# Optimization experiments

Hardware: AMD Instinct MI355X
Metric: run time of the kernel (lower is better)

## Reference

```python
import jax, jax.numpy as jnp
import numpy as np
import math

B, SES, SEQ, H, K = 16, 16, 64, 512, 32
L = SES * SEQ


def setup_inputs() -> dict:
    key = jax.random.key(0)
    ks = jax.random.split(key, 16)
    s = 1.0 / math.sqrt(H)
    return {
        "user_emb": jax.random.normal(ks[0], (B, H), jnp.float32),
        "item_emb": jax.random.normal(ks[1], (B, SES, SEQ, H), jnp.float32),
        "mask": jnp.zeros((B, L, K), jnp.float32),
        "index": jax.random.randint(ks[2], (L, K), 0, L, jnp.int64),
        "Wq": jax.random.normal(ks[3], (H, H), jnp.float32) * s,
        "bq": jnp.zeros((H,), jnp.float32),
        "Wk": jax.random.normal(ks[4], (H, H), jnp.float32) * s,
        "bk": jnp.zeros((H,), jnp.float32),
        "Wv": jax.random.normal(ks[5], (H, H), jnp.float32) * s,
        "bv": jnp.zeros((H,), jnp.float32),
        "Wd": jax.random.normal(ks[6], (H, H), jnp.float32) * s,
        "bd": jnp.zeros((H,), jnp.float32),
        "ln_g": jnp.ones((H,), jnp.float32),
        "ln_b": jnp.zeros((H,), jnp.float32),
    }


def reference(user_emb, item_emb, mask, index, Wq, bq, Wk, bk, Wv, bv, Wd, bd, ln_g, ln_b):
    b, ses, seq, h = item_emb.shape
    l = ses * seq
    item_flat = item_emb.reshape(b, l, h)
    q = user_emb @ Wq.T + bq                       # [B, H]
    k = item_flat @ Wk.T + bk                      # [B, L, H]
    v = item_flat @ Wv.T + bv                      # [B, L, H]
    # scalar query against all L keys, scaled by sqrt(hidden_size)
    scores = jnp.einsum("bh,blh->bl", q, k) / math.sqrt(h)
    scores = scores[:, index] + mask               # gather -> [B, L, K]
    w = jax.nn.softmax(scores, axis=-1)            # [B, L, K]
    vg = v[:, index, :]                            # gather -> [B, L, K, H]
    attn_out = jnp.einsum("blk,blkh->blh", w, vg)  # [B, L, H]
    dense = attn_out @ Wd.T + bd
    x = dense + item_flat                          # residual (dropout = identity, eval)
    mu = jnp.mean(x, axis=-1, keepdims=True)
    var = jnp.var(x, axis=-1, keepdims=True)
    y = (x - mu) / jnp.sqrt(var + 1e-12) * ln_g + ln_b
    return y.reshape(b, ses, seq, h)
```

## Files before the change

kernel.cpp:

```cpp
#include <hip/hip_runtime.h>
#include <math.h>

constexpr int HD   = 512;
constexpr int LL   = 1024;
constexpr int MT   = 16384;
constexpr int KNBR = 32;
constexpr float SCL = 0.04419417382415922f;

typedef __attribute__((ext_vector_type(8))) short  bf16x8;
typedef __attribute__((ext_vector_type(4))) float  f32x4;
typedef __attribute__((ext_vector_type(8))) unsigned short us8;

__device__ inline float b2f(unsigned short u) {
    union { unsigned int i; float f; } v; v.i = (unsigned int)u << 16; return v.f;
}
__device__ inline float b2f_lo(unsigned int u) {
    union { unsigned int i; float f; } v; v.i = u << 16; return v.f;
}
__device__ inline float b2f_hi(unsigned int u) {
    union { unsigned int i; float f; } v; v.i = u & 0xffff0000u; return v.f;
}
__device__ inline unsigned short f2b(float x) {
    union { float f; unsigned int u; } v; v.f = x;
    unsigned int r = v.u + 0x7fff + ((v.u >> 16) & 1);
    return (unsigned short)(r >> 16);
}

__global__ __launch_bounds__(256) void conv_bf(
    const float* __restrict__ s, unsigned short* __restrict__ d, int n)
{
    const int i = (blockIdx.x * 256 + threadIdx.x) * 4;
    if (i < n) {
        float4 v = *(const float4*)&s[i];
        ushort4 o;
        o.x = f2b(v.x); o.y = f2b(v.y); o.z = f2b(v.z); o.w = f2b(v.w);
        *(ushort4*)&d[i] = o;
    }
}

__global__ __launch_bounds__(256) void conv_w3(
    const float* __restrict__ Wk, const float* __restrict__ Wv,
    const float* __restrict__ Wd, unsigned short* __restrict__ Wkv,
    unsigned short* __restrict__ Wdb)
{
    const int n = HD*HD;
    const int i = (blockIdx.x * 256 + threadIdx.x) * 4;
    const float* s; unsigned short* d; int off;
    if (i < n)            { s = Wk; d = Wkv;     off = i; }
    else if (i < 2*n)     { s = Wv; d = Wkv + n; off = i - n; }
    else                  { s = Wd; d = Wdb;     off = i - 2*n; }
    float4 v = *(const float4*)&s[off];
    ushort4 o;
    o.x = f2b(v.x); o.y = f2b(v.y); o.z = f2b(v.z); o.w = f2b(v.w);
    *(ushort4*)&d[off] = o;
}

__global__ __launch_bounds__(256) void gp_q(
    const float* __restrict__ u, const float* __restrict__ Wq,
    const float* __restrict__ bq, float* __restrict__ q)
{
    const int wid  = blockIdx.x * 4 + (threadIdx.x >> 6);
    const int lane = threadIdx.x & 63;
    const int b = wid >> 9, h = wid & 511;
    const float* ur = &u[b*HD + lane*8];
    const float* wr = &Wq[(size_t)h*HD + lane*8];
    const float4 u0 = *(const float4*)ur,     u1 = *(const float4*)(ur+4);
    const float4 w0 = *(const float4*)wr,     w1 = *(const float4*)(wr+4);
    float acc = u0.x*w0.x + u0.y*w0.y + u0.z*w0.z + u0.w*w0.w
              + u1.x*w1.x + u1.y*w1.y + u1.z*w1.z + u1.w*w1.w;
    #pragma unroll
    for (int off = 32; off; off >>= 1) acc += __shfl_down(acc, off);
    if (lane == 0) q[b*HD + h] = acc + bq[h];
}

__global__ __launch_bounds__(256) void scores_init(
    const float* __restrict__ q, const float* __restrict__ bk,
    float* __restrict__ scores)
{
    const int b = blockIdx.x, tid = threadIdx.x;
    float p = q[b*HD + tid]*bk[tid] + q[b*HD + tid + 256]*bk[tid + 256];
    #pragma unroll
    for (int off = 32; off; off >>= 1) p += __shfl_down(p, off);
    __shared__ float sp[4];
    if ((tid & 63) == 0) sp[tid >> 6] = p;
    __syncthreads();
    const float s = (sp[0] + sp[1] + sp[2] + sp[3]) * SCL;
    float4 o = {s, s, s, s};
    *(float4*)&scores[b*LL + tid*4] = o;
}

__global__ __launch_bounds__(256) void gemm_kv(
    const unsigned short* __restrict__ A, const unsigned short* __restrict__ W,
    const float* __restrict__ q, const float* __restrict__ bv,
    float* __restrict__ scores, unsigned short* __restrict__ v_bf)
{
    __shared__ unsigned short As[128 * 32];
    __shared__ unsigned short Bs[128 * 32];

    const int tid  = threadIdx.x;
    const int wave = tid >> 6, lane = tid & 63;
    const int wm = (wave >> 1) * 64;
    const int wn = (wave & 1)  * 64;
    const int row0 = blockIdx.x * 128;
    const int col0 = blockIdx.y * 128;

    const int lrr = lane >> 2;
    const int cc  = lane & 3;
    int st_row[2], st_gchunk[2];
    #pragma unroll
    for (int t = 0; t < 2; t++) {
        const int m = wave*32 + t*16 + lrr;
        st_row[t]    = m;
        st_gchunk[t] = cc ^ ((m >> 1) & 3);
    }

    const int fr   = lane & 15;
    const int quad = lane >> 4;

    f32x4 acc[4][4];
    #pragma unroll
    for (int i = 0; i < 4; i++)
        #pragma unroll
        for (int j = 0; j < 4; j++)
            acc[i][j] = (f32x4){0.f, 0.f, 0.f, 0.f};

    int a_off[4], b_off[4];
    #pragma unroll
    for (int i = 0; i < 4; i++) {
        const int m = wm + i*16 + fr;
        a_off[i] = m*32 + ((quad ^ ((m >> 1) & 3)) << 3);
        const int n = wn + i*16 + fr;
        b_off[i] = n*32 + ((quad ^ ((n >> 1) & 3)) << 3);
    }

    for (int k0 = 0; k0 < HD; k0 += 32) {
        #pragma unroll
        for (int t = 0; t < 2; t++) {
            const int m = st_row[t];
            const unsigned short* ga = &A[(size_t)(row0 + m)*HD + k0 + st_gchunk[t]*8];
            __builtin_amdgcn_global_load_lds(
                (const __attribute__((address_space(1))) void*)ga,
                (__attribute__((address_space(3))) void*)&As[(wave*32 + t*16)*32],
                16, 0, 0);
            const unsigned short* gw = &W[(size_t)(col0 + m)*HD + k0 + st_gchunk[t]*8];
            __builtin_amdgcn_global_load_lds(
                (const __attribute__((address_space(1))) void*)gw,
                (__attribute__((address_space(3))) void*)&Bs[(wave*32 + t*16)*32],
                16, 0, 0);
        }
        __syncthreads();

        bf16x8 af[4], bfr[4];
        #pragma unroll
        for (int i = 0; i < 4; i++) {
            af[i]  = *(const bf16x8*)&As[a_off[i]];
            bfr[i] = *(const bf16x8*)&Bs[b_off[i]];
        }
        #pragma unroll
        for (int i = 0; i < 4; i++)
            #pragma unroll
            for (int j = 0; j < 4; j++)
                acc[i][j] = __builtin_amdgcn_mfma_f32_16x16x32_bf16(
                    af[i], bfr[j], acc[i][j], 0, 0, 0);
        __syncthreads();
    }

    if (col0 < HD) {
        const int b = row0 >> 10;
        float qv[4];
        #pragma unroll
        for (int j = 0; j < 4; j++)
            qv[j] = q[b*HD + col0 + wn + j*16 + fr];
        #pragma unroll
        for (int i = 0; i < 4; i++) {
            #pragma unroll
            for (int r = 0; r < 4; r++) {
                float p = acc[i][0][r]*qv[0] + acc[i][1][r]*qv[1]
                        + acc[i][2][r]*qv[2] + acc[i][3][r]*qv[3];
                #pragma unroll
                for (int off = 1; off < 16; off <<= 1) p += __shfl_xor(p, off);
                if (fr == 0)
                    atomicAdd(&scores[row0 + wm + i*16 + quad*4 + r], p * SCL);
            }
        }
    } else {
        #pragma unroll
        for (int j = 0; j < 4; j++) {
            const int col = col0 - HD + wn + j*16 + fr;
            const float bb = bv[col];
            #pragma unroll
            for (int i = 0; i < 4; i++) {
                #pragma unroll
                for (int r = 0; r < 4; r++) {
                    const int row = row0 + wm + i*16 + quad*4 + r;
                    v_bf[(size_t)row*HD + col] = f2b(acc[i][j][r] + bb);
                }
            }
        }
    }
}

__global__ __launch_bounds__(256) void gp_attn(
    const float* __restrict__ scores, const int* __restrict__ index,
    const float* __restrict__ mask, const unsigned short* __restrict__ v,
    unsigned short* __restrict__ attn)
{
    const int m = blockIdx.x * 4 + (threadIdx.x >> 6);
    const int lane = threadIdx.x & 63;
    const int b = m >> 10, l = m & 1023;

    const int t = lane & 31;
    const int idx = index[l*KNBR + t];
    const float s = scores[b*LL + idx] + mask[(size_t)m*KNBR + t];

    float mx = s;
    #pragma unroll
    for (int off = 16; off; off >>= 1) mx = fmaxf(mx, __shfl_xor(mx, off));
    const float e = __expf(s - mx);
    float sum = e;
    #pragma unroll
    for (int off = 16; off; off >>= 1) sum += __shfl_xor(sum, off);
    const float w = e / sum;

    const unsigned short* vbase = v + (size_t)(b << 10) * HD + lane*8;
    float a[8] = {};
    #pragma unroll 8
    for (int t2 = 0; t2 < KNBR; t2++) {
        const int   it = __shfl(idx, t2);
        const float wt = __shfl(w,   t2);
        const uint4 pv = *(const uint4*)(vbase + (size_t)it*HD);
        a[0] += wt * b2f_lo(pv.x); a[1] += wt * b2f_hi(pv.x);
        a[2] += wt * b2f_lo(pv.y); a[3] += wt * b2f_hi(pv.y);
        a[4] += wt * b2f_lo(pv.z); a[5] += wt * b2f_hi(pv.z);
        a[6] += wt * b2f_lo(pv.w); a[7] += wt * b2f_hi(pv.w);
    }
    uint4 o;
    o.x = (unsigned int)f2b(a[0]) | ((unsigned int)f2b(a[1]) << 16);
    o.y = (unsigned int)f2b(a[2]) | ((unsigned int)f2b(a[3]) << 16);
    o.z = (unsigned int)f2b(a[4]) | ((unsigned int)f2b(a[5]) << 16);
    o.w = (unsigned int)f2b(a[6]) | ((unsigned int)f2b(a[7]) << 16);
    *(uint4*)&attn[(size_t)m*HD + lane*8] = o;
}

__global__ __launch_bounds__(256) void dense_ln(
    const unsigned short* __restrict__ A,
    const unsigned short* __restrict__ W,
    const float* __restrict__ bd, const unsigned short* __restrict__ res,
    const float* __restrict__ ln_g, const float* __restrict__ ln_b,
    float* __restrict__ out)
{
    __shared__ unsigned short As[32 * 32];
    __shared__ unsigned short Bs[512 * 32];
    __shared__ float g_s[HD], lb_s[HD];
    __shared__ float rsum[4][32], rsq[4][32];

    const int tid  = threadIdx.x;
    const int wave = tid >> 6, lane = tid & 63;
    const int row0 = blockIdx.x * 32;

    {
        const int i = tid * 2;
        *(float2*)&g_s[i]  = *(const float2*)&ln_g[i];
        *(float2*)&lb_s[i] = *(const float2*)&ln_b[i];
    }

    const int lrr = lane >> 2;
    const int cc  = lane & 3;
    const int fr   = lane & 15;
    const int quad = lane >> 4;

    f32x4 acc[2][8];
    #pragma unroll
    for (int i = 0; i < 2; i++)
        #pragma unroll
        for (int j = 0; j < 8; j++)
            acc[i][j] = (f32x4){0.f, 0.f, 0.f, 0.f};

    int a_off[2], b_off[8];
    #pragma unroll
    for (int i = 0; i < 2; i++) {
        const int m = i*16 + fr;
        a_off[i] = m*32 + ((quad ^ ((m >> 1) & 3)) << 3);
    }
    #pragma unroll
    for (int j = 0; j < 8; j++) {
        const int n = wave*128 + j*16 + fr;
        b_off[j] = n*32 + ((quad ^ ((n >> 1) & 3)) << 3);
    }

    for (int k0 = 0; k0 < HD; k0 += 32) {
        #pragma unroll
        for (int t = 0; t < 8; t++) {
            const int n = wave*128 + t*16 + lrr;
            const int gch = cc ^ ((n >> 1) & 3);
            const unsigned short* gw = &W[(size_t)n*HD + k0 + gch*8];
            __builtin_amdgcn_global_load_lds(
                (const __attribute__((address_space(1))) void*)gw,
                (__attribute__((address_space(3))) void*)&Bs[(wave*128 + t*16)*32],
                16, 0, 0);
        }
        if (wave < 2) {
            const int m = wave*16 + lrr;
            const int gch = cc ^ ((m >> 1) & 3);
            const unsigned short* ga = &A[(size_t)(row0 + m)*HD + k0 + gch*8];
            __builtin_amdgcn_global_load_lds(
                (const __attribute__((address_space(1))) void*)ga,
                (__attribute__((address_space(3))) void*)&As[(wave*16)*32],
                16, 0, 0);
        }
        __syncthreads();

        bf16x8 af[2], bfr[8];
        #pragma unroll
        for (int i = 0; i < 2; i++) af[i] = *(const bf16x8*)&As[a_off[i]];
        #pragma unroll
        for (int j = 0; j < 8; j++) bfr[j] = *(const bf16x8*)&Bs[b_off[j]];
        #pragma unroll
        for (int i = 0; i < 2; i++)
            #pragma unroll
            for (int j = 0; j < 8; j++)
                acc[i][j] = __builtin_amdgcn_mfma_f32_16x16x32_bf16(
                    af[i], bfr[j], acc[i][j], 0, 0, 0);
        __syncthreads();
    }

    float bdv[8];
    #pragma unroll
    for (int j = 0; j < 8; j++) bdv[j] = bd[wave*128 + j*16 + fr];

    float s1[2][4], s2[2][4];
    #pragma unroll
    for (int i = 0; i < 2; i++) {
        #pragma unroll
        for (int r = 0; r < 4; r++) {
            const int lrow = i*16 + quad*4 + r;
            const size_t gr = (size_t)(row0 + lrow) * HD;
            float a1 = 0.f, a2 = 0.f;
            #pragma unroll
            for (int j = 0; j < 8; j++) {
                const int col = wave*128 + j*16 + fr;
                float val = acc[i][j][r] + bdv[j] + b2f(res[gr + col]);
                acc[i][j][r] = val;
                a1 += val; a2 += val*val;
            }
            #pragma unroll
            for (int off = 1; off < 16; off <<= 1) {
                a1 += __shfl_xor(a1, off);
                a2 += __shfl_xor(a2, off);
            }
            s1[i][r] = a1; s2[i][r] = a2;
            if (fr == 0) { rsum[wave][lrow] = a1; rsq[wave][lrow] = a2; }
        }
    }
    __syncthreads();

    #pragma unroll
    for (int i = 0; i < 2; i++) {
        #pragma unroll
        for (int r = 0; r < 4; r++) {
            const int lrow = i*16 + quad*4 + r;
            const float tot  = rsum[0][lrow] + rsum[1][lrow] + rsum[2][lrow] + rsum[3][lrow];
            const float tot2 = rsq[0][lrow]  + rsq[1][lrow]  + rsq[2][lrow]  + rsq[3][lrow];
            const float mu  = tot * (1.f/HD);
            const float var = tot2 * (1.f/HD) - mu*mu;
            const float inv = rsqrtf(var + 1e-12f);
            const size_t gr = (size_t)(row0 + lrow) * HD;
            #pragma unroll
            for (int j = 0; j < 8; j++) {
                const int col = wave*128 + j*16 + fr;
                out[gr + col] = (acc[i][j][r] - mu)*inv*g_s[col] + lb_s[col];
            }
        }
    }
}

extern "C" void kernel_launch(void* const* d_in, const int* in_sizes, int n_in,
                              void* d_out, int out_size, void* d_ws, size_t ws_size,
                              hipStream_t stream) {
    const float* user_emb = (const float*)d_in[0];
    const float* item_emb = (const float*)d_in[1];
    const float* mask     = (const float*)d_in[2];
    const int*   index    = (const int*)  d_in[3];
    const float* Wq = (const float*)d_in[4];  const float* bq = (const float*)d_in[5];
    const float* Wk = (const float*)d_in[6];  const float* bk = (const float*)d_in[7];
    const float* Wv = (const float*)d_in[8];  const float* bv = (const float*)d_in[9];
    const float* Wd = (const float*)d_in[10]; const float* bd = (const float*)d_in[11];
    const float* ln_g = (const float*)d_in[12];
    const float* ln_b = (const float*)d_in[13];

    float* out = (float*)d_out;

    char* p = (char*)d_ws;
    unsigned short* item_bf = (unsigned short*)p; p += (size_t)MT*HD*2;
    unsigned short* v_bf    = (unsigned short*)p; p += (size_t)MT*HD*2;
    unsigned short* attn_bf = (unsigned short*)p; p += (size_t)MT*HD*2;
    unsigned short* Wkv_bf  = (unsigned short*)p; p += (size_t)2*HD*HD*2;
    unsigned short* Wd_bf   = (unsigned short*)p; p += (size_t)HD*HD*2;
    float* q      = (float*)p; p += 16*HD*4;
    float* scores = (float*)p; p += MT*4;

    conv_bf<<<MT*HD/4/256, 256, 0, stream>>>(item_emb, item_bf, MT*HD);
    conv_w3<<<3*HD*HD/4/256, 256, 0, stream>>>(Wk, Wv, Wd, Wkv_bf, Wd_bf);

    gp_q<<<2048, 256, 0, stream>>>(user_emb, Wq, bq, q);
    scores_init<<<16, 256, 0, stream>>>(q, bk, scores);

    dim3 gkv(MT/128, 8);
    gemm_kv<<<gkv, 256, 0, stream>>>(item_bf, Wkv_bf, q, bv, scores, v_bf);

    gp_attn<<<MT/4, 256, 0, stream>>>(scores, index, mask, v_bf, attn_bf);

    dense_ln<<<MT/32, 256, 0, stream>>>(attn_bf, Wd_bf, bd, item_bf,
                                        ln_g, ln_b, out);
}
```

Measured before the change: 202.9 us.

## Fuse prep kernels into one launch and fuse gather-attention into dense+LayerNorm

Merges the four setup kernels (item/weight bf16 conversion, q projection, score init) into one launch. The score-init blocks recompute q redundantly so they do not depend on the q blocks in the same launch. The gather-attention output is now computed per 32-row tile straight into shared memory inside the dense+LayerNorm kernel, which removes the attn_bf global round trip and one launch. gemm_kv's grid is transposed so consecutive blocks share the same row tile. In exchange, the fused kernel uses more LDS per block, which may lower occupancy, and the score-init blocks add redundant Wq reads.

```diff
diff --git a/kernel.cpp b/kernel.cpp
--- a/kernel.cpp
+++ b/kernel.cpp
@@ -9,7 +9,6 @@
 
 typedef __attribute__((ext_vector_type(8))) short  bf16x8;
 typedef __attribute__((ext_vector_type(4))) float  f32x4;
-typedef __attribute__((ext_vector_type(8))) unsigned short us8;
 
 __device__ inline float b2f(unsigned short u) {
     union { unsigned int i; float f; } v; v.i = (unsigned int)u << 16; return v.f;
@@ -26,67 +25,86 @@
     return (unsigned short)(r >> 16);
 }
 
-__global__ __launch_bounds__(256) void conv_bf(
-    const float* __restrict__ s, unsigned short* __restrict__ d, int n)
+constexpr int PB_CONV_I = 8192;
+constexpr int PB_CONV_W = 768;
+constexpr int PB_Q      = 2048;
+constexpr int PB_SINIT  = 16;
+
+__global__ __launch_bounds__(256) void prep(
+    const float* __restrict__ item, const float* __restrict__ Wk,
+    const float* __restrict__ Wv, const float* __restrict__ Wd,
+    const float* __restrict__ u, const float* __restrict__ Wq,
+    const float* __restrict__ bq, const float* __restrict__ bk,
+    unsigned short* __restrict__ item_bf, unsigned short* __restrict__ Wkv_bf,
+    unsigned short* __restrict__ Wd_bf, float* __restrict__ q,
+    float* __restrict__ scores)
 {
-    const int i = (blockIdx.x * 256 + threadIdx.x) * 4;
-    if (i < n) {
-        float4 v = *(const float4*)&s[i];
+    const int blk = blockIdx.x, tid = threadIdx.x;
+
+    if (blk < PB_CONV_I) {
+        const int i = blk * 1024 + tid * 4;
+        float4 v = *(const float4*)&item[i];
         ushort4 o;
         o.x = f2b(v.x); o.y = f2b(v.y); o.z = f2b(v.z); o.w = f2b(v.w);
-        *(ushort4*)&d[i] = o;
-    }
-}
-
-__global__ __launch_bounds__(256) void conv_w3(
-    const float* __restrict__ Wk, const float* __restrict__ Wv,
-    const float* __restrict__ Wd, unsigned short* __restrict__ Wkv,
-    unsigned short* __restrict__ Wdb)
-{
-    const int n = HD*HD;
-    const int i = (blockIdx.x * 256 + threadIdx.x) * 4;
-    const float* s; unsigned short* d; int off;
-    if (i < n)            { s = Wk; d = Wkv;     off = i; }
-    else if (i < 2*n)     { s = Wv; d = Wkv + n; off = i - n; }
-    else                  { s = Wd; d = Wdb;     off = i - 2*n; }
-    float4 v = *(const float4*)&s[off];
-    ushort4 o;
-    o.x = f2b(v.x); o.y = f2b(v.y); o.z = f2b(v.z); o.w = f2b(v.w);
-    *(ushort4*)&d[off] = o;
-}
-
-__global__ __launch_bounds__(256) void gp_q(
-    const float* __restrict__ u, const float* __restrict__ Wq,
-    const float* __restrict__ bq, float* __restrict__ q)
-{
-    const int wid  = blockIdx.x * 4 + (threadIdx.x >> 6);
-    const int lane = threadIdx.x & 63;
-    const int b = wid >> 9, h = wid & 511;
-    const float* ur = &u[b*HD + lane*8];
-    const float* wr = &Wq[(size_t)h*HD + lane*8];
-    const float4 u0 = *(const float4*)ur,     u1 = *(const float4*)(ur+4);
-    const float4 w0 = *(const float4*)wr,     w1 = *(const float4*)(wr+4);
-    float acc = u0.x*w0.x + u0.y*w0.y + u0.z*w0.z + u0.w*w0.w
-              + u1.x*w1.x + u1.y*w1.y + u1.z*w1.z + u1.w*w1.w;
-    #pragma unroll
-    for (int off = 32; off; off >>= 1) acc += __shfl_down(acc, off);
-    if (lane == 0) q[b*HD + h] = acc + bq[h];
-}
-
-__global__ __launch_bounds__(256) void scores_init(
-    const float* __restrict__ q, const float* __restrict__ bk,
-    float* __restrict__ scores)
-{
-    const int b = blockIdx.x, tid = threadIdx.x;
-    float p = q[b*HD + tid]*bk[tid] + q[b*HD + tid + 256]*bk[tid + 256];
-    #pragma unroll
-    for (int off = 32; off; off >>= 1) p += __shfl_down(p, off);
-    __shared__ float sp[4];
-    if ((tid & 63) == 0) sp[tid >> 6] = p;
-    __syncthreads();
-    const float s = (sp[0] + sp[1] + sp[2] + sp[3]) * SCL;
-    float4 o = {s, s, s, s};
-    *(float4*)&scores[b*LL + tid*4] = o;
+        *(ushort4*)&item_bf[i] = o;
+        return;
+    }
+    if (blk < PB_CONV_I + PB_CONV_W) {
+        const int n = HD*HD;
+        const int i = (blk - PB_CONV_I) * 1024 + tid * 4;
+        const float* s; unsigned short* d; int off;
+        if (i < n)        { s = Wk; d = Wkv_bf;     off = i; }
+        else if (i < 2*n) { s = Wv; d = Wkv_bf + n; off = i - n; }
+        else              { s = Wd; d = Wd_bf;      off = i - 2*n; }
+        float4 v = *(const float4*)&s[off];
+        ushort4 o;
+        o.x = f2b(v.x); o.y = f2b(v.y); o.z = f2b(v.z); o.w = f2b(v.w);
+        *(ushort4*)&d[off] = o;
+        return;
+    }
+    if (blk < PB_CONV_I + PB_CONV_W + PB_Q) {
+        const int wid  = (blk - PB_CONV_I - PB_CONV_W) * 4 + (tid >> 6);
+        const int lane = tid & 63;
+        const int b = wid >> 9, h = wid & 511;
+        const float* ur = &u[b*HD + lane*8];
+        const float* wr = &Wq[(size_t)h*HD + lane*8];
+        const float4 u0 = *(const float4*)ur, u1 = *(const float4*)(ur+4);
+        const float4 w0 = *(const float4*)wr, w1 = *(const float4*)(wr+4);
+        float acc = u0.x*w0.x + u0.y*w0.y + u0.z*w0.z + u0.w*w0.w
+                  + u1.x*w1.x + u1.y*w1.y + u1.z*w1.z + u1.w*w1.w;
+        #pragma unroll
+        for (int off = 32; off; off >>= 1) acc += __shfl_down(acc, off);
+        if (lane == 0) q[b*HD + h] = acc + bq[h];
+        return;
+    }
+    {
+        __shared__ float us[HD];
+        __shared__ float sp[4];
+        const int b = blk - PB_CONV_I - PB_CONV_W - PB_Q;
+        us[tid]       = u[b*HD + tid];
+        us[tid + 256] = u[b*HD + tid + 256];
+        __syncthreads();
+        float contrib = 0.f;
+        #pragma unroll
+        for (int hb = 0; hb < 2; hb++) {
+            const int h = tid + hb*256;
+            const float* wr = &Wq[(size_t)h*HD];
+            float acc = 0.f;
+            for (int j = 0; j < HD; j += 4) {
+                float4 w4 = *(const float4*)&wr[j];
+                float4 u4 = *(const float4*)&us[j];
+                acc += u4.x*w4.x + u4.y*w4.y + u4.z*w4.z + u4.w*w4.w;
+            }
+            contrib += (acc + bq[h]) * bk[h];
+        }
+        #pragma unroll
+        for (int off = 32; off; off >>= 1) contrib += __shfl_down(contrib, off);
+        if ((tid & 63) == 0) sp[tid >> 6] = contrib;
+        __syncthreads();
+        const float s = (sp[0] + sp[1] + sp[2] + sp[3]) * SCL;
+        float4 o = {s, s, s, s};
+        *(float4*)&scores[b*LL + tid*4] = o;
+    }
 }
 
 __global__ __launch_bounds__(256) void gemm_kv(
@@ -101,8 +119,8 @@
     const int wave = tid >> 6, lane = tid & 63;
     const int wm = (wave >> 1) * 64;
     const int wn = (wave & 1)  * 64;
-    const int row0 = blockIdx.x * 128;
-    const int col0 = blockIdx.y * 128;
+    const int row0 = blockIdx.y * 128;
+    const int col0 = blockIdx.x * 128;
 
     const int lrr = lane >> 2;
     const int cc  = lane & 3;
@@ -200,56 +218,17 @@
     }
 }
 
-__global__ __launch_bounds__(256) void gp_attn(
+constexpr int ASTR = HD + 8;
+
+__global__ __launch_bounds__(256) void attn_dense_ln(
     const float* __restrict__ scores, const int* __restrict__ index,
     const float* __restrict__ mask, const unsigned short* __restrict__ v,
-    unsigned short* __restrict__ attn)
-{
-    const int m = blockIdx.x * 4 + (threadIdx.x >> 6);
-    const int lane = threadIdx.x & 63;
-    const int b = m >> 10, l = m & 1023;
-
-    const int t = lane & 31;
-    const int idx = index[l*KNBR + t];
-    const float s = scores[b*LL + idx] + mask[(size_t)m*KNBR + t];
-
-    float mx = s;
-    #pragma unroll
-    for (int off = 16; off; off >>= 1) mx = fmaxf(mx, __shfl_xor(mx, off));
-    const float e = __expf(s - mx);
-    float sum = e;
-    #pragma unroll
-    for (int off = 16; off; off >>= 1) sum += __shfl_xor(sum, off);
-    const float w = e / sum;
-
-    const unsigned short* vbase = v + (size_t)(b << 10) * HD + lane*8;
-    float a[8] = {};
-    #pragma unroll 8
-    for (int t2 = 0; t2 < KNBR; t2++) {
-        const int   it = __shfl(idx, t2);
-        const float wt = __shfl(w,   t2);
-        const uint4 pv = *(const uint4*)(vbase + (size_t)it*HD);
-        a[0] += wt * b2f_lo(pv.x); a[1] += wt * b2f_hi(pv.x);
-        a[2] += wt * b2f_lo(pv.y); a[3] += wt * b2f_hi(pv.y);
-        a[4] += wt * b2f_lo(pv.z); a[5] += wt * b2f_hi(pv.z);
-        a[6] += wt * b2f_lo(pv.w); a[7] += wt * b2f_hi(pv.w);
-    }
-    uint4 o;
-    o.x = (unsigned int)f2b(a[0]) | ((unsigned int)f2b(a[1]) << 16);
-    o.y = (unsigned int)f2b(a[2]) | ((unsigned int)f2b(a[3]) << 16);
-    o.z = (unsigned int)f2b(a[4]) | ((unsigned int)f2b(a[5]) << 16);
-    o.w = (unsigned int)f2b(a[6]) | ((unsigned int)f2b(a[7]) << 16);
-    *(uint4*)&attn[(size_t)m*HD + lane*8] = o;
-}
-
-__global__ __launch_bounds__(256) void dense_ln(
-    const unsigned short* __restrict__ A,
     const unsigned short* __restrict__ W,
     const float* __restrict__ bd, const unsigned short* __restrict__ res,
     const float* __restrict__ ln_g, const float* __restrict__ ln_b,
     float* __restrict__ out)
 {
-    __shared__ unsigned short As[32 * 32];
+    __shared__ unsigned short As2[32 * ASTR];
     __shared__ unsigned short Bs[512 * 32];
     __shared__ float g_s[HD], lb_s[HD];
     __shared__ float rsum[4][32], rsq[4][32];
@@ -264,8 +243,47 @@
         *(float2*)&lb_s[i] = *(const float2*)&ln_b[i];
     }
 
-    const int lrr = lane >> 2;
-    const int cc  = lane & 3;
+    const int t31 = lane & 31;
+    #pragma unroll
+    for (int rr = 0; rr < 8; rr++) {
+        const int lrow = wave*8 + rr;
+        const int m = row0 + lrow;
+        const int b = m >> 10, l = m & 1023;
+
+        const int idx = index[l*KNBR + t31];
+        const float s = scores[b*LL + idx] + mask[(size_t)m*KNBR + t31];
+        float mx = s;
+        #pragma unroll
+        for (int off = 16; off; off >>= 1) mx = fmaxf(mx, __shfl_xor(mx, off));
+        const float e = __expf(s - mx);
+        float sum = e;
+        #pragma unroll
+        for (int off = 16; off; off >>= 1) sum += __shfl_xor(sum, off);
+        const float w = e / sum;
+
+        const unsigned short* vbase = v + (size_t)(b << 10) * HD + lane*8;
+        float a[8] = {};
+        #pragma unroll 8
+        for (int t2 = 0; t2 < KNBR; t2++) {
+            const int   it = __shfl(idx, t2);
+            const float wt = __shfl(w,   t2);
+            const uint4 pv = *(const uint4*)(vbase + (size_t)it*HD);
+            a[0] += wt * b2f_lo(pv.x); a[1] += wt * b2f_hi(pv.x);
+            a[2] += wt * b2f_lo(pv.y); a[3] += wt * b2f_hi(pv.y);
+            a[4] += wt * b2f_lo(pv.z); a[5] += wt * b2f_hi(pv.z);
+            a[6] += wt * b2f_lo(pv.w); a[7] += wt * b2f_hi(pv.w);
+        }
+        uint4 o;
+        o.x = (unsigned int)f2b(a[0]) | ((unsigned int)f2b(a[1]) << 16);
+        o.y = (unsigned int)f2b(a[2]) | ((unsigned int)f2b(a[3]) << 16);
+        o.z = (unsigned int)f2b(a[4]) | ((unsigned int)f2b(a[5]) << 16);
+        o.w = (unsigned int)f2b(a[6]) | ((unsigned int)f2b(a[7]) << 16);
+        *(uint4*)&As2[lrow*ASTR + lane*8] = o;
+    }
+    __syncthreads();
+
+    const int lrr  = lane >> 2;
+    const int cc   = lane & 3;
     const int fr   = lane & 15;
     const int quad = lane >> 4;
 
@@ -276,17 +294,16 @@
         for (int j = 0; j < 8; j++)
             acc[i][j] = (f32x4){0.f, 0.f, 0.f, 0.f};
 
-    int a_off[2], b_off[8];
-    #pragma unroll
-    for (int i = 0; i < 2; i++) {
-        const int m = i*16 + fr;
-        a_off[i] = m*32 + ((quad ^ ((m >> 1) & 3)) << 3);
-    }
+    int b_off[8];
     #pragma unroll
     for (int j = 0; j < 8; j++) {
         const int n = wave*128 + j*16 + fr;
         b_off[j] = n*32 + ((quad ^ ((n >> 1) & 3)) << 3);
     }
+    int a_base[2];
+    #pragma unroll
+    for (int i = 0; i < 2; i++)
+        a_base[i] = (i*16 + fr)*ASTR + quad*8;
 
     for (int k0 = 0; k0 < HD; k0 += 32) {
         #pragma unroll
@@ -299,20 +316,11 @@
                 (__attribute__((address_space(3))) void*)&Bs[(wave*128 + t*16)*32],
                 16, 0, 0);
         }
-        if (wave < 2) {
-            const int m = wave*16 + lrr;
-            const int gch = cc ^ ((m >> 1) & 3);
-            const unsigned short* ga = &A[(size_t)(row0 + m)*HD + k0 + gch*8];
-            __builtin_amdgcn_global_load_lds(
-                (const __attribute__((address_space(1))) void*)ga,
-                (__attribute__((address_space(3))) void*)&As[(wave*16)*32],
-                16, 0, 0);
-        }
         __syncthreads();
 
         bf16x8 af[2], bfr[8];
         #pragma unroll
-        for (int i = 0; i < 2; i++) af[i] = *(const bf16x8*)&As[a_off[i]];
+        for (int i = 0; i < 2; i++) af[i] = *(const bf16x8*)&As2[a_base[i] + k0];
         #pragma unroll
         for (int j = 0; j < 8; j++) bfr[j] = *(const bf16x8*)&Bs[b_off[j]];
         #pragma unroll
@@ -328,7 +336,6 @@
     #pragma unroll
     for (int j = 0; j < 8; j++) bdv[j] = bd[wave*128 + j*16 + fr];
 
-    float s1[2][4], s2[2][4];
     #pragma unroll
     for (int i = 0; i < 2; i++) {
         #pragma unroll
@@ -348,7 +355,6 @@
                 a1 += __shfl_xor(a1, off);
                 a2 += __shfl_xor(a2, off);
             }
-            s1[i][r] = a1; s2[i][r] = a2;
             if (fr == 0) { rsum[wave][lrow] = a1; rsq[wave][lrow] = a2; }
         }
     }
@@ -393,23 +399,19 @@
     char* p = (char*)d_ws;
     unsigned short* item_bf = (unsigned short*)p; p += (size_t)MT*HD*2;
     unsigned short* v_bf    = (unsigned short*)p; p += (size_t)MT*HD*2;
-    unsigned short* attn_bf = (unsigned short*)p; p += (size_t)MT*HD*2;
     unsigned short* Wkv_bf  = (unsigned short*)p; p += (size_t)2*HD*HD*2;
     unsigned short* Wd_bf   = (unsigned short*)p; p += (size_t)HD*HD*2;
     float* q      = (float*)p; p += 16*HD*4;
     float* scores = (float*)p; p += MT*4;
 
-    conv_bf<<<MT*HD/4/256, 256, 0, stream>>>(item_emb, item_bf, MT*HD);
-    conv_w3<<<3*HD*HD/4/256, 256, 0, stream>>>(Wk, Wv, Wd, Wkv_bf, Wd_bf);
-
-    gp_q<<<2048, 256, 0, stream>>>(user_emb, Wq, bq, q);
-    scores_init<<<16, 256, 0, stream>>>(q, bk, scores);
-
-    dim3 gkv(MT/128, 8);
-    gemm_kv<<<gkv, 256, 0, stream>>>(item_bf, Wkv_bf, q, bv, scores, v_bf);
-
-    gp_attn<<<MT/4, 256, 0, stream>>>(scores, index, mask, v_bf, attn_bf);
-
-    dense_ln<<<MT/32, 256, 0, stream>>>(attn_bf, Wd_bf, bd, item_bf,
-                                        ln_g, ln_b, out);
-}
+    prep<<<PB_CONV_I + PB_CONV_W + PB_Q + PB_SINIT, 256, 0, stream>>>(
+        item_emb, Wk, Wv, Wd, user_emb, Wq, bq, bk,
+        item_bf, Wkv_bf, Wd_bf, q, scores);
+
+    gemm_kv<<<dim3(8, 128), 256, 0, stream>>>(item_bf, Wkv_bf, q, bv,
+                                              scores, v_bf);
+
+    attn_dense_ln<<<MT/32, 256, 0, stream>>>(scores, index, mask, v_bf,
+                                             Wd_bf, bd, item_bf,
+                                             ln_g, ln_b, out);
+}
```

After: 253.7 us. 25.0% more time.

## Fold query into Wk so key projection GEMM becomes a GEMV

Applied to the files above, without the earlier changes.

Scores are now computed as item · (Wkᵀq) plus a bias term, with r = Wkᵀq precomputed per batch. The K half of the fused KV GEMM goes away, and with it the atomicAdd score reduction. The conversion and q/r kernels are merged into one prep launch, and a separate GEMV kernel computes the scores. This removes half of the large GEMM's FLOPs and the Wk conversion, at the cost of an extra pass over item_bf and a serial per-batch Wk matvec in 16 blocks.

```diff
diff --git a/kernel.cpp b/kernel.cpp
--- a/kernel.cpp
+++ b/kernel.cpp
@@ -9,7 +9,6 @@
 
 typedef __attribute__((ext_vector_type(8))) short  bf16x8;
 typedef __attribute__((ext_vector_type(4))) float  f32x4;
-typedef __attribute__((ext_vector_type(8))) unsigned short us8;
 
 __device__ inline float b2f(unsigned short u) {
     union { unsigned int i; float f; } v; v.i = (unsigned int)u << 16; return v.f;
@@ -26,73 +25,105 @@
     return (unsigned short)(r >> 16);
 }
 
-__global__ __launch_bounds__(256) void conv_bf(
-    const float* __restrict__ s, unsigned short* __restrict__ d, int n)
+constexpr int PB_CONV_I = 8192;
+constexpr int PB_CONV_W = 512;
+constexpr int PB_QR     = 16;
+
+__global__ __launch_bounds__(256) void prep(
+    const float* __restrict__ item, const float* __restrict__ Wv,
+    const float* __restrict__ Wd, const float* __restrict__ u,
+    const float* __restrict__ Wq, const float* __restrict__ bq,
+    const float* __restrict__ Wk, const float* __restrict__ bk,
+    unsigned short* __restrict__ item_bf, unsigned short* __restrict__ Wv_bf,
+    unsigned short* __restrict__ Wd_bf, float* __restrict__ rbuf,
+    float* __restrict__ s0buf)
 {
-    const int i = (blockIdx.x * 256 + threadIdx.x) * 4;
-    if (i < n) {
-        float4 v = *(const float4*)&s[i];
+    const int blk = blockIdx.x, tid = threadIdx.x;
+
+    if (blk < PB_CONV_I) {
+        const int i = blk * 1024 + tid * 4;
+        float4 v = *(const float4*)&item[i];
         ushort4 o;
         o.x = f2b(v.x); o.y = f2b(v.y); o.z = f2b(v.z); o.w = f2b(v.w);
-        *(ushort4*)&d[i] = o;
-    }
-}
-
-__global__ __launch_bounds__(256) void conv_w3(
-    const float* __restrict__ Wk, const float* __restrict__ Wv,
-    const float* __restrict__ Wd, unsigned short* __restrict__ Wkv,
-    unsigned short* __restrict__ Wdb)
+        *(ushort4*)&item_bf[i] = o;
+        return;
+    }
+    if (blk < PB_CONV_I + PB_CONV_W) {
+        const int n = HD*HD;
+        const int i = (blk - PB_CONV_I) * 1024 + tid * 4;
+        const float* s; unsigned short* d; int off;
+        if (i < n) { s = Wv; d = Wv_bf; off = i; }
+        else       { s = Wd; d = Wd_bf; off = i - n; }
+        float4 v = *(const float4*)&s[off];
+        ushort4 o;
+        o.x = f2b(v.x); o.y = f2b(v.y); o.z = f2b(v.z); o.w = f2b(v.w);
+        *(ushort4*)&d[off] = o;
+        return;
+    }
+    {
+        __shared__ float us[HD];
+        __shared__ float qs[HD];
+        __shared__ float sp[4];
+        const int b = blk - PB_CONV_I - PB_CONV_W;
+        us[tid]       = u[b*HD + tid];
+        us[tid + 256] = u[b*HD + tid + 256];
+        __syncthreads();
+        #pragma unroll
+        for (int hb = 0; hb < 2; hb++) {
+            const int h = tid + hb*256;
+            const float* wr = &Wq[(size_t)h*HD];
+            float acc = 0.f;
+            for (int j = 0; j < HD; j += 4) {
+                float4 w4 = *(const float4*)&wr[j];
+                float4 u4 = *(const float4*)&us[j];
+                acc += u4.x*w4.x + u4.y*w4.y + u4.z*w4.z + u4.w*w4.w;
+            }
+            qs[h] = acc + bq[h];
+        }
+        __syncthreads();
+        float r0 = 0.f, r1 = 0.f;
+        const int c0 = tid * 2;
+        #pragma unroll 8
+        for (int h = 0; h < HD; h++) {
+            const float2 w2 = *(const float2*)&Wk[(size_t)h*HD + c0];
+            const float qh = qs[h];
+            r0 += qh * w2.x; r1 += qh * w2.y;
+        }
+        rbuf[b*HD + c0]     = r0 * SCL;
+        rbuf[b*HD + c0 + 1] = r1 * SCL;
+        float p = qs[tid]*bk[tid] + qs[tid+256]*bk[tid+256];
+        #pragma unroll
+        for (int off = 32; off; off >>= 1) p += __shfl_down(p, off);
+        if ((tid & 63) == 0) sp[tid >> 6] = p;
+        __syncthreads();
+        if (tid == 0) s0buf[b] = (sp[0] + sp[1] + sp[2] + sp[3]) * SCL;
+    }
+}
+
+__global__ __launch_bounds__(256) void gp_scores(
+    const float* __restrict__ rbuf, const float* __restrict__ s0buf,
+    const unsigned short* __restrict__ item_bf, float* __restrict__ scores)
 {
-    const int n = HD*HD;
-    const int i = (blockIdx.x * 256 + threadIdx.x) * 4;
-    const float* s; unsigned short* d; int off;
-    if (i < n)            { s = Wk; d = Wkv;     off = i; }
-    else if (i < 2*n)     { s = Wv; d = Wkv + n; off = i - n; }
-    else                  { s = Wd; d = Wdb;     off = i - 2*n; }
-    float4 v = *(const float4*)&s[off];
-    ushort4 o;
-    o.x = f2b(v.x); o.y = f2b(v.y); o.z = f2b(v.z); o.w = f2b(v.w);
-    *(ushort4*)&d[off] = o;
-}
-
-__global__ __launch_bounds__(256) void gp_q(
-    const float* __restrict__ u, const float* __restrict__ Wq,
-    const float* __restrict__ bq, float* __restrict__ q)
-{
-    const int wid  = blockIdx.x * 4 + (threadIdx.x >> 6);
+    const int m = blockIdx.x * 4 + (threadIdx.x >> 6);
     const int lane = threadIdx.x & 63;
-    const int b = wid >> 9, h = wid & 511;
-    const float* ur = &u[b*HD + lane*8];
-    const float* wr = &Wq[(size_t)h*HD + lane*8];
-    const float4 u0 = *(const float4*)ur,     u1 = *(const float4*)(ur+4);
-    const float4 w0 = *(const float4*)wr,     w1 = *(const float4*)(wr+4);
-    float acc = u0.x*w0.x + u0.y*w0.y + u0.z*w0.z + u0.w*w0.w
-              + u1.x*w1.x + u1.y*w1.y + u1.z*w1.z + u1.w*w1.w;
+    const int b = m >> 10;
+    const unsigned short* ir = &item_bf[(size_t)m*HD + lane*8];
+    const uint4 iv = *(const uint4*)ir;
+    const float* rr = &rbuf[b*HD + lane*8];
+    const float4 r0 = *(const float4*)rr;
+    const float4 r1 = *(const float4*)(rr + 4);
+    float acc = r0.x*b2f_lo(iv.x) + r0.y*b2f_hi(iv.x)
+              + r0.z*b2f_lo(iv.y) + r0.w*b2f_hi(iv.y)
+              + r1.x*b2f_lo(iv.z) + r1.y*b2f_hi(iv.z)
+              + r1.z*b2f_lo(iv.w) + r1.w*b2f_hi(iv.w);
     #pragma unroll
     for (int off = 32; off; off >>= 1) acc += __shfl_down(acc, off);
-    if (lane == 0) q[b*HD + h] = acc + bq[h];
-}
-
-__global__ __launch_bounds__(256) void scores_init(
-    const float* __restrict__ q, const float* __restrict__ bk,
-    float* __restrict__ scores)
-{
-    const int b = blockIdx.x, tid = threadIdx.x;
-    float p = q[b*HD + tid]*bk[tid] + q[b*HD + tid + 256]*bk[tid + 256];
-    #pragma unroll
-    for (int off = 32; off; off >>= 1) p += __shfl_down(p, off);
-    __shared__ float sp[4];
-    if ((tid & 63) == 0) sp[tid >> 6] = p;
-    __syncthreads();
-    const float s = (sp[0] + sp[1] + sp[2] + sp[3]) * SCL;
-    float4 o = {s, s, s, s};
-    *(float4*)&scores[b*LL + tid*4] = o;
-}
-
-__global__ __launch_bounds__(256) void gemm_kv(
+    if (lane == 0) scores[m] = acc + s0buf[b];
+}
+
+__global__ __launch_bounds__(256) void gemm_v(
     const unsigned short* __restrict__ A, const unsigned short* __restrict__ W,
-    const float* __restrict__ q, const float* __restrict__ bv,
-    float* __restrict__ scores, unsigned short* __restrict__ v_bf)
+    const float* __restrict__ bv, unsigned short* __restrict__ v_bf)
 {
     __shared__ unsigned short As[128 * 32];
     __shared__ unsigned short Bs[128 * 32];
@@ -101,8 +132,8 @@
     const int wave = tid >> 6, lane = tid & 63;
     const int wm = (wave >> 1) * 64;
     const int wn = (wave & 1)  * 64;
-    const int row0 = blockIdx.x * 128;
-    const int col0 = blockIdx.y * 128;
+    const int row0 = blockIdx.y * 128;
+    const int col0 = blockIdx.x * 128;
 
     const int lrr = lane >> 2;
     const int cc  = lane & 3;
@@ -165,36 +196,16 @@
         __syncthreads();
     }
 
-    if (col0 < HD) {
-        const int b = row0 >> 10;
-        float qv[4];
-        #pragma unroll
-        for (int j = 0; j < 4; j++)
-            qv[j] = q[b*HD + col0 + wn + j*16 + fr];
+    #pragma unroll
+    for (int j = 0; j < 4; j++) {
+        const int col = col0 + wn + j*16 + fr;
+        const float bb = bv[col];
         #pragma unroll
         for (int i = 0; i < 4; i++) {
             #pragma unroll
             for (int r = 0; r < 4; r++) {
-                float p = acc[i][0][r]*qv[0] + acc[i][1][r]*qv[1]
-                        + acc[i][2][r]*qv[2] + acc[i][3][r]*qv[3];
-                #pragma unroll
-                for (int off = 1; off < 16; off <<= 1) p += __shfl_xor(p, off);
-                if (fr == 0)
-                    atomicAdd(&scores[row0 + wm + i*16 + quad*4 + r], p * SCL);
-            }
-        }
-    } else {
-        #pragma unroll
-        for (int j = 0; j < 4; j++) {
-            const int col = col0 - HD + wn + j*16 + fr;
-            const float bb = bv[col];
-            #pragma unroll
-            for (int i = 0; i < 4; i++) {
-                #pragma unroll
-                for (int r = 0; r < 4; r++) {
-                    const int row = row0 + wm + i*16 + quad*4 + r;
-                    v_bf[(size_t)row*HD + col] = f2b(acc[i][j][r] + bb);
-                }
+                const int row = row0 + wm + i*16 + quad*4 + r;
+                v_bf[(size_t)row*HD + col] = f2b(acc[i][j][r] + bb);
             }
         }
     }
@@ -328,7 +339,6 @@
     #pragma unroll
     for (int j = 0; j < 8; j++) bdv[j] = bd[wave*128 + j*16 + fr];
 
-    float s1[2][4], s2[2][4];
     #pragma unroll
     for (int i = 0; i < 2; i++) {
         #pragma unroll
@@ -348,7 +358,6 @@
                 a1 += __shfl_xor(a1, off);
                 a2 += __shfl_xor(a2, off);
             }
-            s1[i][r] = a1; s2[i][r] = a2;
             if (fr == 0) { rsum[wave][lrow] = a1; rsq[wave][lrow] = a2; }
         }
     }
@@ -394,19 +403,19 @@
     unsigned short* item_bf = (unsigned short*)p; p += (size_t)MT*HD*2;
     unsigned short* v_bf    = (unsigned short*)p; p += (size_t)MT*HD*2;
     unsigned short* attn_bf = (unsigned short*)p; p += (size_t)MT*HD*2;
-    unsigned short* Wkv_bf  = (unsigned short*)p; p += (size_t)2*HD*HD*2;
+    unsigned short* Wv_bf   = (unsigned short*)p; p += (size_t)HD*HD*2;
     unsigned short* Wd_bf   = (unsigned short*)p; p += (size_t)HD*HD*2;
-    float* q      = (float*)p; p += 16*HD*4;
+    float* rbuf   = (float*)p; p += 16*HD*4;
+    float* s0buf  = (float*)p; p += 16*4;
     float* scores = (float*)p; p += MT*4;
 
-    conv_bf<<<MT*HD/4/256, 256, 0, stream>>>(item_emb, item_bf, MT*HD);
-    conv_w3<<<3*HD*HD/4/256, 256, 0, stream>>>(Wk, Wv, Wd, Wkv_bf, Wd_bf);
-
-    gp_q<<<2048, 256, 0, stream>>>(user_emb, Wq, bq, q);
-    scores_init<<<16, 256, 0, stream>>>(q, bk, scores);
-
-    dim3 gkv(MT/128, 8);
-    gemm_kv<<<gkv, 256, 0, stream>>>(item_bf, Wkv_bf, q, bv, scores, v_bf);
+    prep<<<PB_CONV_I + PB_CONV_W + PB_QR, 256, 0, stream>>>(
+        item_emb, Wv, Wd, user_emb, Wq, bq, Wk, bk,
+        item_bf, Wv_bf, Wd_bf, rbuf, s0buf);
+
+    gp_scores<<<MT/4, 256, 0, stream>>>(rbuf, s0buf, item_bf, scores);
+
+    gemm_v<<<dim3(4, 128), 256, 0, stream>>>(item_bf, Wv_bf, bv, v_bf);
 
     gp_attn<<<MT/4, 256, 0, stream>>>(scores, index, mask, v_bf, attn_bf);
 
```

Result: slower. 239.7 us (+18.1%).
